# Kernel optimization log

Hardware: AMD Instinct MI355X
Metric: run time of the kernel (lower is better)

The kernel has to match this reference:

```python
import jax, jax.numpy as jnp
import numpy as np

T, H, E, I, TOP_K = 4096, 1024, 8, 2048, 2
EPS = 1e-05


def setup_inputs() -> dict:
    key = jax.random.key(0)
    ks = jax.random.split(key, 4)
    x = jax.random.normal(ks[0], (T, H), dtype=jnp.float32)
    scale = jnp.ones((H,), dtype=jnp.float32)
    gate_kernel = jax.random.normal(ks[1], (H, E), dtype=jnp.float32) * (1.0 / np.sqrt(H))
    gate_bias = jnp.zeros((E,), dtype=jnp.float32)
    mlp1_weight = jax.random.normal(ks[2], (E, H, 2 * I), dtype=jnp.float32) * (1.0 / np.sqrt(H))
    mlp1_bias = jnp.zeros((E, 2 * I), dtype=jnp.float32)
    mlp2_weight = jax.random.normal(ks[3], (E, I, H), dtype=jnp.float32) * (1.0 / np.sqrt(I))
    mlp2_bias = jnp.zeros((E, H), dtype=jnp.float32)
    return {"x": x, "scale": scale, "gate_kernel": gate_kernel, "gate_bias": gate_bias,
            "mlp1_weight": mlp1_weight, "mlp1_bias": mlp1_bias,
            "mlp2_weight": mlp2_weight, "mlp2_bias": mlp2_bias}


def _rmsnorm(x, scale):
    t = x.astype(jnp.float32)
    rms = jnp.sqrt(jnp.mean(t * t, axis=-1, keepdims=True) + EPS)
    return ((t / rms) * scale).astype(x.dtype)


def reference(x, scale, gate_kernel, gate_bias, mlp1_weight, mlp1_bias, mlp2_weight, mlp2_bias):
    normed = _rmsnorm(x, scale)                                   # [T, H]
    _ = normed @ gate_kernel + gate_bias                          # gate logits (unused: static routing)
    # dense per-token, all-expert MLP: [T,H] x [E,H,2I] -> [T,E,2I]
    hidden = jnp.einsum('th,ehi->tei', normed, mlp1_weight) + mlp1_bias
    gate = jnp.minimum(hidden[..., :I], 7.0)
    linear = jnp.clip(hidden[..., I:], -7.0, 7.0)
    activated = gate * jax.nn.sigmoid(1.702 * gate) * (linear + 1.0)
    expert_out = jnp.einsum('tei,eih->teh', activated, mlp2_weight) + mlp2_bias  # [T,E,H]
    # static uniform routing over the first TOP_K experts
    mix = jnp.where(jnp.arange(E) < TOP_K, 1.0 / TOP_K, 0.0).astype(x.dtype)     # [E]
    fused = jnp.einsum('teh,e->th', expert_out, mix)
    return x + fused
```

## Files before the change

kernel.cpp:

```cpp
#include <hip/hip_runtime.h>
#include <hip/hip_bf16.h>
#include <stdint.h>

#define T_DIM 4096
#define H_DIM 1024
#define I_DIM 2048

typedef __bf16 bf16x8 __attribute__((ext_vector_type(8)));
typedef float f32x4 __attribute__((ext_vector_type(4)));
typedef unsigned short ushort_t;
typedef unsigned short us4 __attribute__((ext_vector_type(4)));

__device__ __forceinline__ unsigned short f32_to_bf16(float f) {
  unsigned int u = __float_as_uint(f);
  u += 0x7fffu + ((u >> 16) & 1u);
  return (unsigned short)(u >> 16);
}

__device__ __forceinline__ void gload_lds16(const void* g, void* l) {
  __builtin_amdgcn_global_load_lds(
      (__attribute__((address_space(1))) void*)(uintptr_t)g,
      (__attribute__((address_space(3))) void*)(unsigned int)(uintptr_t)l,
      16, 0, 0);
}

__device__ __forceinline__ int swz(int L) { return L ^ (((L >> 7) & 7) << 4); }

#define S_BARRIER() asm volatile("s_barrier" ::: "memory")
#define WAITV(n) asm volatile("s_waitcnt vmcnt(" #n ")" ::: "memory")
#define IRFENCE() asm volatile("" ::: "memory")
#define MFMA16(acc, va, vb) \
  acc = __builtin_amdgcn_mfma_f32_16x16x32_bf16(va, vb, acc, 0, 0, 0)

__global__ __launch_bounds__(256) void k_rmsnorm_init(
    const float* __restrict__ x, const float* __restrict__ scale,
    const float* __restrict__ b2, ushort_t* __restrict__ normed,
    float* __restrict__ out) {
  const int row = blockIdx.x, tid = threadIdx.x;
  const float4 v = ((const float4*)(x + (size_t)row * H_DIM))[tid];
  float ss = v.x * v.x + v.y * v.y + v.z * v.z + v.w * v.w;
#pragma unroll
  for (int off = 32; off > 0; off >>= 1) ss += __shfl_xor(ss, off);
  __shared__ float wsum[4];
  if ((tid & 63) == 0) wsum[tid >> 6] = ss;
  __syncthreads();
  const float tot = wsum[0] + wsum[1] + wsum[2] + wsum[3];
  const float inv = rsqrtf(tot * (1.0f / H_DIM) + 1e-5f);
  const float4 sc = ((const float4*)scale)[tid];
  us4 o;
  o.x = f32_to_bf16(v.x * inv * sc.x);
  o.y = f32_to_bf16(v.y * inv * sc.y);
  o.z = f32_to_bf16(v.z * inv * sc.z);
  o.w = f32_to_bf16(v.w * inv * sc.w);
  ((us4*)(normed + (size_t)row * H_DIM))[tid] = o;
  const float4 b0 = ((const float4*)b2)[tid];
  const float4 b1 = ((const float4*)(b2 + H_DIM))[tid];
  float4 ov;
  ov.x = v.x + 0.5f * (b0.x + b1.x);
  ov.y = v.y + 0.5f * (b0.y + b1.y);
  ov.z = v.z + 0.5f * (b0.z + b1.z);
  ov.w = v.w + 0.5f * (b0.w + b1.w);
  ((float4*)(out + (size_t)row * H_DIM))[tid] = ov;
}

__global__ __launch_bounds__(256) void k_transpose_cvt(const float* __restrict__ src,
                                                       ushort_t* __restrict__ dst,
                                                       int R, int C) {
  __shared__ float tile[32][33];
  const size_t eoff = (size_t)blockIdx.z * (size_t)R * (size_t)C;
  src += eoff;
  dst += eoff;
  const int x0 = blockIdx.x * 32, y0 = blockIdx.y * 32;
  const int tx = threadIdx.x & 31, ty = threadIdx.x >> 5;
#pragma unroll
  for (int i = 0; i < 4; ++i)
    tile[ty + 8 * i][tx] = src[(size_t)(y0 + ty + 8 * i) * C + x0 + tx];
  __syncthreads();
#pragma unroll
  for (int i = 0; i < 4; ++i)
    dst[(size_t)(x0 + ty + 8 * i) * R + y0 + tx] = f32_to_bf16(tile[tx][ty + 8 * i]);
}

__global__ __launch_bounds__(256, 2) void k_gemm1(
    const ushort_t* __restrict__ normed, const ushort_t* __restrict__ w1T,
    const float* __restrict__ b1, ushort_t* __restrict__ act) {
  __shared__ __align__(16) ushort_t lds[3][3][4096];
  char* const ldsB = (char*)&lds[0][0][0];
  const int tid = threadIdx.x;
  const int wg = (blockIdx.x & 7) * 128 + (blockIdx.x >> 3);
  const int e = wg >> 9;
  const int rem = wg & 511;
  const int brow = (rem >> 4) * 128;
  const int bcol = (rem & 15) * 128;
  const int lane = tid & 63;
  const int wid = tid >> 6;
  const int wm = wid >> 1, wn = wid & 1;
  const int r16 = lane & 15, kh = lane >> 4;

  const ushort_t* gBase = w1T + ((size_t)e * 2 * I_DIM + bcol) * H_DIM;
  const ushort_t* lBase = w1T + ((size_t)e * 2 * I_DIM + I_DIM + bcol) * H_DIM;

  f32x4 accg[4][4], accl[4][4];
  const f32x4 zf = {0.f, 0.f, 0.f, 0.f};
#pragma unroll
  for (int m = 0; m < 4; ++m)
#pragma unroll
    for (int n = 0; n < 4; ++n) { accg[m][n] = zf; accl[m][n] = zf; }

  const ushort_t* pA[2];
  const ushort_t* pG[2];
  const ushort_t* pL[2];
#pragma unroll
  for (int j = 0; j < 2; ++j) {
    const int u = swz(j * 4096 + tid * 16);
    const int r = u >> 6, c = (u & 63) >> 1;
    pA[j] = normed + (size_t)(brow + r) * H_DIM + c;
    pG[j] = gBase + (size_t)r * H_DIM + c;
    pL[j] = lBase + (size_t)r * H_DIM + c;
  }
  const int ldst0 = (tid & ~63) * 16;

  const int abase = swz((wm * 64 + r16) * 64 + kh * 16);
  const int bbase = 8192 + swz((wn * 64 + r16) * 64 + kh * 16);

  auto stage = [&](int buf) {
#pragma unroll
    for (int j = 0; j < 2; ++j) {
      gload_lds16(pA[j], ldsB + buf * 24576 + j * 4096 + ldst0);
      gload_lds16(pG[j], ldsB + buf * 24576 + 8192 + j * 4096 + ldst0);
      gload_lds16(pL[j], ldsB + buf * 24576 + 16384 + j * 4096 + ldst0);
    }
  };

  bf16x8 a[4], bg[4], bl[4];

#define G1_ADV()                                                              \
  {                                                                           \
    _Pragma("unroll") for (int j = 0; j < 2; ++j) {                           \
      pA[j] += 32; pG[j] += 32; pL[j] += 32;                                  \
    }                                                                         \
  }
#define G1_RD(C)                                                              \
  _Pragma("unroll") for (int m = 0; m < 4; ++m)                               \
      a[m] = *(const bf16x8*)(ldsB + (C) * 24576 + abase + m * 1024);         \
  _Pragma("unroll") for (int n = 0; n < 4; ++n) {                             \
    bg[n] = *(const bf16x8*)(ldsB + (C) * 24576 + bbase + n * 1024);          \
    bl[n] = *(const bf16x8*)(ldsB + (C) * 24576 + bbase + 8192 + n * 1024);   \
  }
#define G1_MFMA()                                                             \
  _Pragma("unroll") for (int m = 0; m < 4; ++m)                               \
      _Pragma("unroll") for (int n = 0; n < 4; ++n) {                         \
    MFMA16(accg[m][n], a[m], bg[n]);                                          \
    MFMA16(accl[m][n], a[m], bl[n]);                                          \
  }
#define G1_STEP(C, N)                                                         \
  {                                                                           \
    G1_RD(C);                                                                 \
    stage(N);                                                                 \
    __builtin_amdgcn_s_setprio(1);                                            \
    G1_MFMA();                                                                \
    __builtin_amdgcn_s_setprio(0);                                            \
    WAITV(6);                                                                 \
    S_BARRIER();                                                              \
    G1_ADV();                                                                 \
  }

  stage(0); IRFENCE();
  G1_ADV();
  stage(1);
  G1_ADV();
  WAITV(6);
  S_BARRIER();

#pragma unroll 1
  for (int it = 0; it < 10; ++it) {
    G1_STEP(0, 2);
    G1_STEP(1, 0);
    G1_STEP(2, 1);
  }
  {
    G1_RD(0);
    G1_MFMA();
    WAITV(0);
    S_BARRIER();
    G1_RD(1);
    G1_MFMA();
  }
#undef G1_STEP
#undef G1_MFMA
#undef G1_RD
#undef G1_ADV

  const float* b1e = b1 + (size_t)e * 2 * I_DIM;
#pragma unroll
  for (int m = 0; m < 4; ++m)
#pragma unroll
    for (int n = 0; n < 4; ++n) {
      const int gcol = bcol + wn * 64 + n * 16 + r16;
      const float bgb = b1e[gcol];
      const float blb = b1e[I_DIM + gcol];
#pragma unroll
      for (int rr = 0; rr < 4; ++rr) {
        const int grow = brow + wm * 64 + m * 16 + kh * 4 + rr;
        const float hg = accg[m][n][rr] + bgb;
        const float hl = accl[m][n][rr] + blb;
        const float g = fminf(hg, 7.f);
        const float l = fminf(fmaxf(hl, -7.f), 7.f);
        const float s = 1.f / (1.f + __expf(-1.702f * g));
        const float av = g * s * (l + 1.f);
        act[((size_t)e * T_DIM + grow) * I_DIM + gcol] = f32_to_bf16(av);
      }
    }
}

__global__ __launch_bounds__(256, 3) void k_gemm2(
    const ushort_t* __restrict__ act, const ushort_t* __restrict__ w2T,
    float* __restrict__ out) {
  __shared__ __align__(16) ushort_t lds[3][2][4096];
  char* const ldsB = (char*)&lds[0][0][0];
  const int tid = threadIdx.x;
  const int wg = (blockIdx.x & 7) * 64 + (blockIdx.x >> 3);
  const int e = wg >> 8;
  const int rem = wg & 255;
  const int brow = (rem >> 3) * 128;
  const int bcol = (rem & 7) * 128;
  const int lane = tid & 63;
  const int wid = tid >> 6;
  const int wm = wid >> 1, wn = wid & 1;
  const int r16 = lane & 15, kh = lane >> 4;

  const ushort_t* aBase = act + ((size_t)e * T_DIM + brow) * I_DIM;
  const ushort_t* bBase = w2T + ((size_t)e * H_DIM + bcol) * I_DIM;

  f32x4 acc[4][4];
  const f32x4 zf = {0.f, 0.f, 0.f, 0.f};
#pragma unroll
  for (int m = 0; m < 4; ++m)
#pragma unroll
    for (int n = 0; n < 4; ++n) acc[m][n] = zf;

  const ushort_t* pA[2];
  const ushort_t* pB[2];
#pragma unroll
  for (int j = 0; j < 2; ++j) {
    const int u = swz(j * 4096 + tid * 16);
    const int r = u >> 6, c = (u & 63) >> 1;
    pA[j] = aBase + (size_t)r * I_DIM + c;
    pB[j] = bBase + (size_t)r * I_DIM + c;
  }
  const int ldst0 = (tid & ~63) * 16;

  const int abase = swz((wm * 64 + r16) * 64 + kh * 16);
  const int bbase = 8192 + swz((wn * 64 + r16) * 64 + kh * 16);

  auto stage = [&](int buf) {
#pragma unroll
    for (int j = 0; j < 2; ++j) {
      gload_lds16(pA[j], ldsB + buf * 16384 + j * 4096 + ldst0);
      gload_lds16(pB[j], ldsB + buf * 16384 + 8192 + j * 4096 + ldst0);
    }
  };

  bf16x8 a[4], b[4];

#define G2_ADV()                                                              \
  {                                                                           \
    _Pragma("unroll") for (int j = 0; j < 2; ++j) { pA[j] += 32; pB[j] += 32; } \
  }
#define G2_RD(C)                                                              \
  _Pragma("unroll") for (int m = 0; m < 4; ++m)                               \
      a[m] = *(const bf16x8*)(ldsB + (C) * 16384 + abase + m * 1024);         \
  _Pragma("unroll") for (int n = 0; n < 4; ++n)                               \
      b[n] = *(const bf16x8*)(ldsB + (C) * 16384 + bbase + n * 1024);
#define G2_MFMA()                                                             \
  _Pragma("unroll") for (int m = 0; m < 4; ++m)                               \
      _Pragma("unroll") for (int n = 0; n < 4; ++n)                           \
          MFMA16(acc[m][n], a[m], b[n]);
#define G2_STEP(C, N)                                                         \
  {                                                                           \
    G2_RD(C);                                                                 \
    stage(N);                                                                 \
    __builtin_amdgcn_s_setprio(1);                                            \
    G2_MFMA();                                                                \
    __builtin_amdgcn_s_setprio(0);                                            \
    WAITV(4);                                                                 \
    S_BARRIER();                                                              \
    G2_ADV();                                                                 \
  }

  stage(0); IRFENCE();
  G2_ADV();
  stage(1);
  G2_ADV();
  WAITV(4);
  S_BARRIER();

#pragma unroll 1
  for (int it = 0; it < 20; ++it) {
    G2_STEP(0, 2);
    G2_STEP(1, 0);
    G2_STEP(2, 1);
  }
  G2_STEP(0, 2);
  G2_STEP(1, 0);
  {
    G2_RD(2);
    G2_MFMA();
    WAITV(0);
    S_BARRIER();
    G2_RD(0);
    G2_MFMA();
  }
#undef G2_STEP
#undef G2_MFMA
#undef G2_RD
#undef G2_ADV

#pragma unroll
  for (int m = 0; m < 4; ++m)
#pragma unroll
    for (int n = 0; n < 4; ++n) {
      const int gcol = bcol + wn * 64 + n * 16 + r16;
#pragma unroll
      for (int rr = 0; rr < 4; ++rr) {
        const int grow = brow + wm * 64 + m * 16 + kh * 4 + rr;
        atomicAdd(&out[(size_t)grow * H_DIM + gcol], 0.5f * acc[m][n][rr]);
      }
    }
}

extern "C" void kernel_launch(void* const* d_in, const int* in_sizes, int n_in,
                              void* d_out, int out_size, void* d_ws, size_t ws_size,
                              hipStream_t stream) {
  const float* x = (const float*)d_in[0];
  const float* scale = (const float*)d_in[1];
  const float* w1 = (const float*)d_in[4];
  const float* b1 = (const float*)d_in[5];
  const float* w2 = (const float*)d_in[6];
  const float* b2 = (const float*)d_in[7];
  float* out = (float*)d_out;

  ushort_t* ws = (ushort_t*)d_ws;
  ushort_t* normed = ws;
  ushort_t* w1T = normed + (size_t)T_DIM * H_DIM;
  ushort_t* w2T = w1T + (size_t)2 * 2 * I_DIM * H_DIM;
  ushort_t* actb = w2T + (size_t)2 * H_DIM * I_DIM;

  k_rmsnorm_init<<<dim3(T_DIM), 256, 0, stream>>>(x, scale, b2, normed, out);
  k_transpose_cvt<<<dim3(2 * I_DIM / 32, H_DIM / 32, 2), 256, 0, stream>>>(
      w1, w1T, H_DIM, 2 * I_DIM);
  k_transpose_cvt<<<dim3(H_DIM / 32, I_DIM / 32, 2), 256, 0, stream>>>(
      w2, w2T, I_DIM, H_DIM);
  k_gemm1<<<dim3(1024), 256, 0, stream>>>(normed, w1T, b1, actb);
  k_gemm2<<<dim3(512), 256, 0, stream>>>(actb, w2T, out);
}
```

Before: 154.4 us.

## Fuse prep kernels, overlap w2 transpose with gemm1, split-K 256x256 gemm2

Merges the RMSnorm/init kernel with the w1 transpose into one launch. The w2 transpose now runs as extra blocks appended to the gemm1 launch, so it can overlap with the GEMM tail. gemm2 is reworked to 512-thread blocks with 256x256 tiles and a split-K of two halves of I, accumulating through the existing atomics. This cuts launch count and idle gaps, but gemm2 now runs only 256 blocks, with larger per-thread accumulators and higher register and LDS pressure.

```diff
diff --git a/kernel.cpp b/kernel.cpp
--- a/kernel.cpp
+++ b/kernel.cpp
@@ -32,45 +32,14 @@
 #define MFMA16(acc, va, vb) \
   acc = __builtin_amdgcn_mfma_f32_16x16x32_bf16(va, vb, acc, 0, 0, 0)
 
-__global__ __launch_bounds__(256) void k_rmsnorm_init(
-    const float* __restrict__ x, const float* __restrict__ scale,
-    const float* __restrict__ b2, ushort_t* __restrict__ normed,
-    float* __restrict__ out) {
-  const int row = blockIdx.x, tid = threadIdx.x;
-  const float4 v = ((const float4*)(x + (size_t)row * H_DIM))[tid];
-  float ss = v.x * v.x + v.y * v.y + v.z * v.z + v.w * v.w;
-#pragma unroll
-  for (int off = 32; off > 0; off >>= 1) ss += __shfl_xor(ss, off);
-  __shared__ float wsum[4];
-  if ((tid & 63) == 0) wsum[tid >> 6] = ss;
-  __syncthreads();
-  const float tot = wsum[0] + wsum[1] + wsum[2] + wsum[3];
-  const float inv = rsqrtf(tot * (1.0f / H_DIM) + 1e-5f);
-  const float4 sc = ((const float4*)scale)[tid];
-  us4 o;
-  o.x = f32_to_bf16(v.x * inv * sc.x);
-  o.y = f32_to_bf16(v.y * inv * sc.y);
-  o.z = f32_to_bf16(v.z * inv * sc.z);
-  o.w = f32_to_bf16(v.w * inv * sc.w);
-  ((us4*)(normed + (size_t)row * H_DIM))[tid] = o;
-  const float4 b0 = ((const float4*)b2)[tid];
-  const float4 b1 = ((const float4*)(b2 + H_DIM))[tid];
-  float4 ov;
-  ov.x = v.x + 0.5f * (b0.x + b1.x);
-  ov.y = v.y + 0.5f * (b0.y + b1.y);
-  ov.z = v.z + 0.5f * (b0.z + b1.z);
-  ov.w = v.w + 0.5f * (b0.w + b1.w);
-  ((float4*)(out + (size_t)row * H_DIM))[tid] = ov;
-}
-
-__global__ __launch_bounds__(256) void k_transpose_cvt(const float* __restrict__ src,
-                                                       ushort_t* __restrict__ dst,
-                                                       int R, int C) {
-  __shared__ float tile[32][33];
-  const size_t eoff = (size_t)blockIdx.z * (size_t)R * (size_t)C;
+__device__ __forceinline__ void transpose_body(const float* __restrict__ src,
+                                               ushort_t* __restrict__ dst,
+                                               int R, int C, int bx, int by,
+                                               int bz, float (*tile)[33]) {
+  const size_t eoff = (size_t)bz * (size_t)R * (size_t)C;
   src += eoff;
   dst += eoff;
-  const int x0 = blockIdx.x * 32, y0 = blockIdx.y * 32;
+  const int x0 = bx * 32, y0 = by * 32;
   const int tx = threadIdx.x & 31, ty = threadIdx.x >> 5;
 #pragma unroll
   for (int i = 0; i < 4; ++i)
@@ -81,13 +50,59 @@
     dst[(size_t)(x0 + ty + 8 * i) * R + y0 + tx] = f32_to_bf16(tile[tx][ty + 8 * i]);
 }
 
-__global__ __launch_bounds__(256, 2) void k_gemm1(
+__global__ __launch_bounds__(256) void k_prep1(
+    const float* __restrict__ x, const float* __restrict__ scale,
+    const float* __restrict__ b2, const float* __restrict__ w1,
+    ushort_t* __restrict__ normed, float* __restrict__ out,
+    ushort_t* __restrict__ w1T) {
+  __shared__ __align__(16) float shm[32][33];
+  const int bid = blockIdx.x;
+  if (bid < T_DIM) {
+    const int row = bid, tid = threadIdx.x;
+    const float4 v = ((const float4*)(x + (size_t)row * H_DIM))[tid];
+    float ss = v.x * v.x + v.y * v.y + v.z * v.z + v.w * v.w;
+#pragma unroll
+    for (int off = 32; off > 0; off >>= 1) ss += __shfl_xor(ss, off);
+    if ((tid & 63) == 0) shm[0][tid >> 6] = ss;
+    __syncthreads();
+    const float tot = shm[0][0] + shm[0][1] + shm[0][2] + shm[0][3];
+    const float inv = rsqrtf(tot * (1.0f / H_DIM) + 1e-5f);
+    const float4 sc = ((const float4*)scale)[tid];
+    us4 o;
+    o.x = f32_to_bf16(v.x * inv * sc.x);
+    o.y = f32_to_bf16(v.y * inv * sc.y);
+    o.z = f32_to_bf16(v.z * inv * sc.z);
+    o.w = f32_to_bf16(v.w * inv * sc.w);
+    ((us4*)(normed + (size_t)row * H_DIM))[tid] = o;
+    const float4 b0 = ((const float4*)b2)[tid];
+    const float4 b1 = ((const float4*)(b2 + H_DIM))[tid];
+    float4 ov;
+    ov.x = v.x + 0.5f * (b0.x + b1.x);
+    ov.y = v.y + 0.5f * (b0.y + b1.y);
+    ov.z = v.z + 0.5f * (b0.z + b1.z);
+    ov.w = v.w + 0.5f * (b0.w + b1.w);
+    ((float4*)(out + (size_t)row * H_DIM))[tid] = ov;
+  } else {
+    const int t = bid - T_DIM;
+    transpose_body(w1, w1T, H_DIM, 2 * I_DIM, t & 127, (t >> 7) & 31, t >> 12,
+                   shm);
+  }
+}
+
+__global__ __launch_bounds__(256, 2) void k_gemm1_tr2(
     const ushort_t* __restrict__ normed, const ushort_t* __restrict__ w1T,
-    const float* __restrict__ b1, ushort_t* __restrict__ act) {
+    const float* __restrict__ b1, ushort_t* __restrict__ act,
+    const float* __restrict__ w2, ushort_t* __restrict__ w2T) {
   __shared__ __align__(16) ushort_t lds[3][3][4096];
   char* const ldsB = (char*)&lds[0][0][0];
+  if (blockIdx.x >= 1024) {
+    const int t = blockIdx.x - 1024;
+    transpose_body(w2, w2T, I_DIM, H_DIM, t & 31, (t >> 5) & 63, t >> 11,
+                   (float(*)[33])ldsB);
+    return;
+  }
   const int tid = threadIdx.x;
-  const int wg = (blockIdx.x & 7) * 128 + (blockIdx.x >> 3);
+  const int wg = ((blockIdx.x & 7) << 7) + (blockIdx.x >> 3);
   const int e = wg >> 9;
   const int rem = wg & 511;
   const int brow = (rem >> 4) * 128;
@@ -213,29 +228,31 @@
     }
 }
 
-__global__ __launch_bounds__(256, 3) void k_gemm2(
+__global__ __launch_bounds__(512, 2) void k_gemm2(
     const ushort_t* __restrict__ act, const ushort_t* __restrict__ w2T,
     float* __restrict__ out) {
-  __shared__ __align__(16) ushort_t lds[3][2][4096];
+  __shared__ __align__(16) ushort_t lds[3][2][8192];
   char* const ldsB = (char*)&lds[0][0][0];
   const int tid = threadIdx.x;
-  const int wg = (blockIdx.x & 7) * 64 + (blockIdx.x >> 3);
-  const int e = wg >> 8;
-  const int rem = wg & 255;
-  const int brow = (rem >> 3) * 128;
-  const int bcol = (rem & 7) * 128;
+  const int bid = blockIdx.x;
+  const int kc = bid >> 6;
+  const int tile = bid & 63;
+  const int e = kc >> 1, ih = kc & 1;
+  const int brow = (tile >> 2) * 256;
+  const int bcol = (tile & 3) * 256;
   const int lane = tid & 63;
   const int wid = tid >> 6;
-  const int wm = wid >> 1, wn = wid & 1;
+  const int wm = wid >> 2;
+  const int wn = wid & 3;
   const int r16 = lane & 15, kh = lane >> 4;
 
-  const ushort_t* aBase = act + ((size_t)e * T_DIM + brow) * I_DIM;
-  const ushort_t* bBase = w2T + ((size_t)e * H_DIM + bcol) * I_DIM;
-
-  f32x4 acc[4][4];
+  const ushort_t* aBase = act + ((size_t)e * T_DIM + brow) * I_DIM + ih * 1024;
+  const ushort_t* bBase = w2T + ((size_t)e * H_DIM + bcol) * I_DIM + ih * 1024;
+
+  f32x4 acc[8][4];
   const f32x4 zf = {0.f, 0.f, 0.f, 0.f};
 #pragma unroll
-  for (int m = 0; m < 4; ++m)
+  for (int m = 0; m < 8; ++m)
 #pragma unroll
     for (int n = 0; n < 4; ++n) acc[m][n] = zf;
 
@@ -243,37 +260,37 @@
   const ushort_t* pB[2];
 #pragma unroll
   for (int j = 0; j < 2; ++j) {
-    const int u = swz(j * 4096 + tid * 16);
+    const int u = swz(j * 8192 + tid * 16);
     const int r = u >> 6, c = (u & 63) >> 1;
     pA[j] = aBase + (size_t)r * I_DIM + c;
     pB[j] = bBase + (size_t)r * I_DIM + c;
   }
   const int ldst0 = (tid & ~63) * 16;
 
-  const int abase = swz((wm * 64 + r16) * 64 + kh * 16);
-  const int bbase = 8192 + swz((wn * 64 + r16) * 64 + kh * 16);
+  const int abase = wm * 8192 + swz(r16 * 64 + kh * 16);
+  const int bbase = 16384 + wn * 4096 + swz(r16 * 64 + kh * 16);
 
   auto stage = [&](int buf) {
 #pragma unroll
     for (int j = 0; j < 2; ++j) {
-      gload_lds16(pA[j], ldsB + buf * 16384 + j * 4096 + ldst0);
-      gload_lds16(pB[j], ldsB + buf * 16384 + 8192 + j * 4096 + ldst0);
+      gload_lds16(pA[j], ldsB + buf * 32768 + j * 8192 + ldst0);
+      gload_lds16(pB[j], ldsB + buf * 32768 + 16384 + j * 8192 + ldst0);
     }
   };
 
-  bf16x8 a[4], b[4];
+  bf16x8 a[8], b[4];
 
 #define G2_ADV()                                                              \
   {                                                                           \
     _Pragma("unroll") for (int j = 0; j < 2; ++j) { pA[j] += 32; pB[j] += 32; } \
   }
 #define G2_RD(C)                                                              \
-  _Pragma("unroll") for (int m = 0; m < 4; ++m)                               \
-      a[m] = *(const bf16x8*)(ldsB + (C) * 16384 + abase + m * 1024);         \
+  _Pragma("unroll") for (int m = 0; m < 8; ++m)                               \
+      a[m] = *(const bf16x8*)(ldsB + (C) * 32768 + abase + m * 1024);         \
   _Pragma("unroll") for (int n = 0; n < 4; ++n)                               \
-      b[n] = *(const bf16x8*)(ldsB + (C) * 16384 + bbase + n * 1024);
+      b[n] = *(const bf16x8*)(ldsB + (C) * 32768 + bbase + n * 1024);
 #define G2_MFMA()                                                             \
-  _Pragma("unroll") for (int m = 0; m < 4; ++m)                               \
+  _Pragma("unroll") for (int m = 0; m < 8; ++m)                               \
       _Pragma("unroll") for (int n = 0; n < 4; ++n)                           \
           MFMA16(acc[m][n], a[m], b[n]);
 #define G2_STEP(C, N)                                                         \
@@ -296,19 +313,17 @@
   S_BARRIER();
 
 #pragma unroll 1
-  for (int it = 0; it < 20; ++it) {
+  for (int it = 0; it < 10; ++it) {
     G2_STEP(0, 2);
     G2_STEP(1, 0);
     G2_STEP(2, 1);
   }
-  G2_STEP(0, 2);
-  G2_STEP(1, 0);
   {
-    G2_RD(2);
+    G2_RD(0);
     G2_MFMA();
     WAITV(0);
     S_BARRIER();
-    G2_RD(0);
+    G2_RD(1);
     G2_MFMA();
   }
 #undef G2_STEP
@@ -317,13 +332,13 @@
 #undef G2_ADV
 
 #pragma unroll
-  for (int m = 0; m < 4; ++m)
+  for (int m = 0; m < 8; ++m)
 #pragma unroll
     for (int n = 0; n < 4; ++n) {
       const int gcol = bcol + wn * 64 + n * 16 + r16;
 #pragma unroll
       for (int rr = 0; rr < 4; ++rr) {
-        const int grow = brow + wm * 64 + m * 16 + kh * 4 + rr;
+        const int grow = brow + wm * 128 + m * 16 + kh * 4 + rr;
         atomicAdd(&out[(size_t)grow * H_DIM + gcol], 0.5f * acc[m][n][rr]);
       }
     }
@@ -346,11 +361,9 @@
   ushort_t* w2T = w1T + (size_t)2 * 2 * I_DIM * H_DIM;
   ushort_t* actb = w2T + (size_t)2 * H_DIM * I_DIM;
 
-  k_rmsnorm_init<<<dim3(T_DIM), 256, 0, stream>>>(x, scale, b2, normed, out);
-  k_transpose_cvt<<<dim3(2 * I_DIM / 32, H_DIM / 32, 2), 256, 0, stream>>>(
-      w1, w1T, H_DIM, 2 * I_DIM);
-  k_transpose_cvt<<<dim3(H_DIM / 32, I_DIM / 32, 2), 256, 0, stream>>>(
-      w2, w2T, I_DIM, H_DIM);
-  k_gemm1<<<dim3(1024), 256, 0, stream>>>(normed, w1T, b1, actb);
-  k_gemm2<<<dim3(512), 256, 0, stream>>>(actb, w2T, out);
-}
+  k_prep1<<<dim3(T_DIM + 8192), 256, 0, stream>>>(x, scale, b2, w1, normed,
+                                                  out, w1T);
+  k_gemm1_tr2<<<dim3(1024 + 4096), 256, 0, stream>>>(normed, w1T, b1, actb,
+                                                     w2, w2T);
+  k_gemm2<<<dim3(256), 512, 0, stream>>>(actb, w2T, out);
+}
```

Result: slower. 172.0 us (+11.4%).

## Concatenate expert K dimension in GEMM2, drop atomics, fuse prep kernels

Applied to the files above, without the earlier changes.

The activation and W2 layouts are rearranged so both experts are concatenated along K (4096). GEMM2 becomes a single 128x64-tile GEMM that writes x + bias + 0.5*acc directly instead of doing atomicAdd. This removes the atomic traffic and the separate output-init pass. The rmsnorm and both weight transposes are merged into one launch, with a wider 64x64 vectorized transpose. In exchange GEMM2 uses smaller N tiles, so each A tile is reused less and per-block work changes.

```diff
diff --git a/kernel.cpp b/kernel.cpp
--- a/kernel.cpp
+++ b/kernel.cpp
@@ -5,11 +5,13 @@
 #define T_DIM 4096
 #define H_DIM 1024
 #define I_DIM 2048
+#define KCAT 4096
 
 typedef __bf16 bf16x8 __attribute__((ext_vector_type(8)));
 typedef float f32x4 __attribute__((ext_vector_type(4)));
 typedef unsigned short ushort_t;
 typedef unsigned short us4 __attribute__((ext_vector_type(4)));
+typedef unsigned short us8 __attribute__((ext_vector_type(8)));
 
 __device__ __forceinline__ unsigned short f32_to_bf16(float f) {
   unsigned int u = __float_as_uint(f);
@@ -32,53 +34,70 @@
 #define MFMA16(acc, va, vb) \
   acc = __builtin_amdgcn_mfma_f32_16x16x32_bf16(va, vb, acc, 0, 0, 0)
 
-__global__ __launch_bounds__(256) void k_rmsnorm_init(
+__device__ __forceinline__ void transpose_body64(const float* __restrict__ src,
+                                                 ushort_t* __restrict__ dst,
+                                                 int sC, int dR, int bx, int by,
+                                                 float (*tile)[65]) {
+  const int x0 = bx * 64, y0 = by * 64;
+  const int tid = threadIdx.x;
+  const int lcol4 = tid & 15, lrow = tid >> 4;
+#pragma unroll
+  for (int i = 0; i < 4; ++i) {
+    const int r = lrow + 16 * i;
+    const float4 v = ((const float4*)(src + (size_t)(y0 + r) * sC + x0))[lcol4];
+    tile[r][lcol4 * 4 + 0] = v.x;
+    tile[r][lcol4 * 4 + 1] = v.y;
+    tile[r][lcol4 * 4 + 2] = v.z;
+    tile[r][lcol4 * 4 + 3] = v.w;
+  }
+  __syncthreads();
+  const int slotr = tid & 7, lcol = tid >> 3;
+#pragma unroll
+  for (int i = 0; i < 2; ++i) {
+    const int c = lcol + 32 * i;
+    us8 o;
+#pragma unroll
+    for (int j = 0; j < 8; ++j) o[j] = f32_to_bf16(tile[slotr * 8 + j][c]);
+    *(us8*)(dst + (size_t)(x0 + c) * dR + y0 + slotr * 8) = o;
+  }
+}
+
+__global__ __launch_bounds__(256) void k_prep1(
     const float* __restrict__ x, const float* __restrict__ scale,
-    const float* __restrict__ b2, ushort_t* __restrict__ normed,
-    float* __restrict__ out) {
-  const int row = blockIdx.x, tid = threadIdx.x;
-  const float4 v = ((const float4*)(x + (size_t)row * H_DIM))[tid];
-  float ss = v.x * v.x + v.y * v.y + v.z * v.z + v.w * v.w;
-#pragma unroll
-  for (int off = 32; off > 0; off >>= 1) ss += __shfl_xor(ss, off);
-  __shared__ float wsum[4];
-  if ((tid & 63) == 0) wsum[tid >> 6] = ss;
-  __syncthreads();
-  const float tot = wsum[0] + wsum[1] + wsum[2] + wsum[3];
-  const float inv = rsqrtf(tot * (1.0f / H_DIM) + 1e-5f);
-  const float4 sc = ((const float4*)scale)[tid];
-  us4 o;
-  o.x = f32_to_bf16(v.x * inv * sc.x);
-  o.y = f32_to_bf16(v.y * inv * sc.y);
-  o.z = f32_to_bf16(v.z * inv * sc.z);
-  o.w = f32_to_bf16(v.w * inv * sc.w);
-  ((us4*)(normed + (size_t)row * H_DIM))[tid] = o;
-  const float4 b0 = ((const float4*)b2)[tid];
-  const float4 b1 = ((const float4*)(b2 + H_DIM))[tid];
-  float4 ov;
-  ov.x = v.x + 0.5f * (b0.x + b1.x);
-  ov.y = v.y + 0.5f * (b0.y + b1.y);
-  ov.z = v.z + 0.5f * (b0.z + b1.z);
-  ov.w = v.w + 0.5f * (b0.w + b1.w);
-  ((float4*)(out + (size_t)row * H_DIM))[tid] = ov;
-}
-
-__global__ __launch_bounds__(256) void k_transpose_cvt(const float* __restrict__ src,
-                                                       ushort_t* __restrict__ dst,
-                                                       int R, int C) {
-  __shared__ float tile[32][33];
-  const size_t eoff = (size_t)blockIdx.z * (size_t)R * (size_t)C;
-  src += eoff;
-  dst += eoff;
-  const int x0 = blockIdx.x * 32, y0 = blockIdx.y * 32;
-  const int tx = threadIdx.x & 31, ty = threadIdx.x >> 5;
-#pragma unroll
-  for (int i = 0; i < 4; ++i)
-    tile[ty + 8 * i][tx] = src[(size_t)(y0 + ty + 8 * i) * C + x0 + tx];
-  __syncthreads();
-#pragma unroll
-  for (int i = 0; i < 4; ++i)
-    dst[(size_t)(x0 + ty + 8 * i) * R + y0 + tx] = f32_to_bf16(tile[tx][ty + 8 * i]);
+    const float* __restrict__ w1, const float* __restrict__ w2,
+    ushort_t* __restrict__ normed, ushort_t* __restrict__ w1T,
+    ushort_t* __restrict__ w2c) {
+  __shared__ __align__(16) float shm[64][65];
+  const int bid = blockIdx.x;
+  if (bid < T_DIM) {
+    const int row = bid, tid = threadIdx.x;
+    const float4 v = ((const float4*)(x + (size_t)row * H_DIM))[tid];
+    float ss = v.x * v.x + v.y * v.y + v.z * v.z + v.w * v.w;
+#pragma unroll
+    for (int off = 32; off > 0; off >>= 1) ss += __shfl_xor(ss, off);
+    if ((tid & 63) == 0) shm[0][tid >> 6] = ss;
+    __syncthreads();
+    const float tot = shm[0][0] + shm[0][1] + shm[0][2] + shm[0][3];
+    const float inv = rsqrtf(tot * (1.0f / H_DIM) + 1e-5f);
+    const float4 sc = ((const float4*)scale)[tid];
+    us4 o;
+    o.x = f32_to_bf16(v.x * inv * sc.x);
+    o.y = f32_to_bf16(v.y * inv * sc.y);
+    o.z = f32_to_bf16(v.z * inv * sc.z);
+    o.w = f32_to_bf16(v.w * inv * sc.w);
+    ((us4*)(normed + (size_t)row * H_DIM))[tid] = o;
+  } else if (bid < T_DIM + 2048) {
+    const int t = bid - T_DIM;
+    const int e = t >> 10;
+    transpose_body64(w1 + (size_t)e * H_DIM * 2 * I_DIM,
+                     w1T + (size_t)e * 2 * I_DIM * H_DIM, 2 * I_DIM, H_DIM,
+                     t & 63, (t >> 6) & 15, shm);
+  } else {
+    const int t = bid - T_DIM - 2048;
+    const int e = t >> 9;
+    transpose_body64(w2 + (size_t)e * I_DIM * H_DIM, w2c + (size_t)e * I_DIM,
+                     H_DIM, KCAT, t & 15, (t >> 4) & 31, shm);
+  }
 }
 
 __global__ __launch_bounds__(256, 2) void k_gemm1(
@@ -87,7 +106,7 @@
   __shared__ __align__(16) ushort_t lds[3][3][4096];
   char* const ldsB = (char*)&lds[0][0][0];
   const int tid = threadIdx.x;
-  const int wg = (blockIdx.x & 7) * 128 + (blockIdx.x >> 3);
+  const int wg = ((blockIdx.x & 7) << 7) + (blockIdx.x >> 3);
   const int e = wg >> 9;
   const int rem = wg & 511;
   const int brow = (rem >> 4) * 128;
@@ -208,73 +227,71 @@
         const float l = fminf(fmaxf(hl, -7.f), 7.f);
         const float s = 1.f / (1.f + __expf(-1.702f * g));
         const float av = g * s * (l + 1.f);
-        act[((size_t)e * T_DIM + grow) * I_DIM + gcol] = f32_to_bf16(av);
+        act[(size_t)grow * KCAT + e * I_DIM + gcol] = f32_to_bf16(av);
       }
     }
 }
 
 __global__ __launch_bounds__(256, 3) void k_gemm2(
-    const ushort_t* __restrict__ act, const ushort_t* __restrict__ w2T,
+    const ushort_t* __restrict__ act, const ushort_t* __restrict__ w2c,
+    const float* __restrict__ x, const float* __restrict__ b2,
     float* __restrict__ out) {
-  __shared__ __align__(16) ushort_t lds[3][2][4096];
-  char* const ldsB = (char*)&lds[0][0][0];
+  __shared__ __align__(16) ushort_t lds[3][6144];
+  char* const ldsB = (char*)&lds[0][0];
   const int tid = threadIdx.x;
-  const int wg = (blockIdx.x & 7) * 64 + (blockIdx.x >> 3);
-  const int e = wg >> 8;
-  const int rem = wg & 255;
-  const int brow = (rem >> 3) * 128;
-  const int bcol = (rem & 7) * 128;
+  const int wg = ((blockIdx.x & 7) << 6) + (blockIdx.x >> 3);
+  const int brow = (wg >> 4) * 128;
+  const int bcol = (wg & 15) * 64;
   const int lane = tid & 63;
   const int wid = tid >> 6;
   const int wm = wid >> 1, wn = wid & 1;
   const int r16 = lane & 15, kh = lane >> 4;
 
-  const ushort_t* aBase = act + ((size_t)e * T_DIM + brow) * I_DIM;
-  const ushort_t* bBase = w2T + ((size_t)e * H_DIM + bcol) * I_DIM;
-
-  f32x4 acc[4][4];
+  const ushort_t* aBase = act + (size_t)brow * KCAT;
+  const ushort_t* bBase = w2c + (size_t)bcol * KCAT;
+
+  f32x4 acc[4][2];
   const f32x4 zf = {0.f, 0.f, 0.f, 0.f};
 #pragma unroll
   for (int m = 0; m < 4; ++m)
 #pragma unroll
-    for (int n = 0; n < 4; ++n) acc[m][n] = zf;
+    for (int n = 0; n < 2; ++n) acc[m][n] = zf;
 
   const ushort_t* pA[2];
-  const ushort_t* pB[2];
-#pragma unroll
-  for (int j = 0; j < 2; ++j) {
-    const int u = swz(j * 4096 + tid * 16);
-    const int r = u >> 6, c = (u & 63) >> 1;
-    pA[j] = aBase + (size_t)r * I_DIM + c;
-    pB[j] = bBase + (size_t)r * I_DIM + c;
+  const ushort_t* pB;
+  {
+#pragma unroll
+    for (int j = 0; j < 2; ++j) {
+      const int u = swz(j * 4096 + tid * 16);
+      pA[j] = aBase + (size_t)(u >> 6) * KCAT + ((u & 63) >> 1);
+    }
+    const int u = swz(tid * 16);
+    pB = bBase + (size_t)(u >> 6) * KCAT + ((u & 63) >> 1);
   }
   const int ldst0 = (tid & ~63) * 16;
 
   const int abase = swz((wm * 64 + r16) * 64 + kh * 16);
-  const int bbase = 8192 + swz((wn * 64 + r16) * 64 + kh * 16);
+  const int bbase = 8192 + swz((wn * 32 + r16) * 64 + kh * 16);
 
   auto stage = [&](int buf) {
 #pragma unroll
-    for (int j = 0; j < 2; ++j) {
-      gload_lds16(pA[j], ldsB + buf * 16384 + j * 4096 + ldst0);
-      gload_lds16(pB[j], ldsB + buf * 16384 + 8192 + j * 4096 + ldst0);
-    }
+    for (int j = 0; j < 2; ++j)
+      gload_lds16(pA[j], ldsB + buf * 12288 + j * 4096 + ldst0);
+    gload_lds16(pB, ldsB + buf * 12288 + 8192 + ldst0);
   };
 
-  bf16x8 a[4], b[4];
-
-#define G2_ADV()                                                              \
-  {                                                                           \
-    _Pragma("unroll") for (int j = 0; j < 2; ++j) { pA[j] += 32; pB[j] += 32; } \
-  }
+  bf16x8 a[4], b[2];
+
+#define G2_ADV() \
+  { pA[0] += 32; pA[1] += 32; pB += 32; }
 #define G2_RD(C)                                                              \
   _Pragma("unroll") for (int m = 0; m < 4; ++m)                               \
-      a[m] = *(const bf16x8*)(ldsB + (C) * 16384 + abase + m * 1024);         \
-  _Pragma("unroll") for (int n = 0; n < 4; ++n)                               \
-      b[n] = *(const bf16x8*)(ldsB + (C) * 16384 + bbase + n * 1024);
+      a[m] = *(const bf16x8*)(ldsB + (C) * 12288 + abase + m * 1024);         \
+  _Pragma("unroll") for (int n = 0; n < 2; ++n)                               \
+      b[n] = *(const bf16x8*)(ldsB + (C) * 12288 + bbase + n * 1024);
 #define G2_MFMA()                                                             \
   _Pragma("unroll") for (int m = 0; m < 4; ++m)                               \
-      _Pragma("unroll") for (int n = 0; n < 4; ++n)                           \
+      _Pragma("unroll") for (int n = 0; n < 2; ++n)                           \
           MFMA16(acc[m][n], a[m], b[n]);
 #define G2_STEP(C, N)                                                         \
   {                                                                           \
@@ -283,7 +300,7 @@
     __builtin_amdgcn_s_setprio(1);                                            \
     G2_MFMA();                                                                \
     __builtin_amdgcn_s_setprio(0);                                            \
-    WAITV(4);                                                                 \
+    WAITV(3);                                                                 \
     S_BARRIER();                                                              \
     G2_ADV();                                                                 \
   }
@@ -292,23 +309,21 @@
   G2_ADV();
   stage(1);
   G2_ADV();
-  WAITV(4);
+  WAITV(3);
   S_BARRIER();
 
 #pragma unroll 1
-  for (int it = 0; it < 20; ++it) {
+  for (int it = 0; it < 42; ++it) {
     G2_STEP(0, 2);
     G2_STEP(1, 0);
     G2_STEP(2, 1);
   }
-  G2_STEP(0, 2);
-  G2_STEP(1, 0);
   {
-    G2_RD(2);
+    G2_RD(0);
     G2_MFMA();
     WAITV(0);
     S_BARRIER();
-    G2_RD(0);
+    G2_RD(1);
     G2_MFMA();
   }
 #undef G2_STEP
@@ -319,12 +334,14 @@
 #pragma unroll
   for (int m = 0; m < 4; ++m)
 #pragma unroll
-    for (int n = 0; n < 4; ++n) {
-      const int gcol = bcol + wn * 64 + n * 16 + r16;
+    for (int n = 0; n < 2; ++n) {
+      const int gcol = bcol + wn * 32 + n * 16 + r16;
+      const float bb = 0.5f * (b2[gcol] + b2[H_DIM + gcol]);
 #pragma unroll
       for (int rr = 0; rr < 4; ++rr) {
         const int grow = brow + wm * 64 + m * 16 + kh * 4 + rr;
-        atomicAdd(&out[(size_t)grow * H_DIM + gcol], 0.5f * acc[m][n][rr]);
+        out[(size_t)grow * H_DIM + gcol] =
+            x[(size_t)grow * H_DIM + gcol] + 0.5f * acc[m][n][rr] + bb;
       }
     }
 }
@@ -343,14 +360,11 @@
   ushort_t* ws = (ushort_t*)d_ws;
   ushort_t* normed = ws;
   ushort_t* w1T = normed + (size_t)T_DIM * H_DIM;
-  ushort_t* w2T = w1T + (size_t)2 * 2 * I_DIM * H_DIM;
-  ushort_t* actb = w2T + (size_t)2 * H_DIM * I_DIM;
-
-  k_rmsnorm_init<<<dim3(T_DIM), 256, 0, stream>>>(x, scale, b2, normed, out);
-  k_transpose_cvt<<<dim3(2 * I_DIM / 32, H_DIM / 32, 2), 256, 0, stream>>>(
-      w1, w1T, H_DIM, 2 * I_DIM);
-  k_transpose_cvt<<<dim3(H_DIM / 32, I_DIM / 32, 2), 256, 0, stream>>>(
-      w2, w2T, I_DIM, H_DIM);
+  ushort_t* w2c = w1T + (size_t)2 * 2 * I_DIM * H_DIM;
+  ushort_t* actb = w2c + (size_t)H_DIM * KCAT;
+
+  k_prep1<<<dim3(T_DIM + 2048 + 1024), 256, 0, stream>>>(
+      x, scale, w1, w2, normed, w1T, w2c);
   k_gemm1<<<dim3(1024), 256, 0, stream>>>(normed, w1T, b1, actb);
-  k_gemm2<<<dim3(512), 256, 0, stream>>>(actb, w2T, out);
-}
+  k_gemm2<<<dim3(512), 256, 0, stream>>>(actb, w2c, x, b2, out);
+}
```

Measured after the change: 148.3 us. -4.0%, faster.
